# Optimization experiments

Hardware: AMD Instinct MI355X
Metric: run time of the kernel (lower is better)

The kernel has to match this reference:

```python
import jax, jax.numpy as jnp
import numpy as np

N = 20000
E = 320000
NEG_SLOPE = 0.2
BN_EPS = 1e-5


def _segment_softmax(e, dst, n):
    # e: [E, H] attention logits, dst: [E] destination node ids
    m = jax.ops.segment_max(e, dst, num_segments=n)           # [N, H]
    ex = jnp.exp(e - m[dst])                                   # [E, H]
    s = jax.ops.segment_sum(ex, dst, num_segments=n)          # [N, H]
    return ex / s[dst]


def gat_conv(x, src, dst, W, a_src, a_dst, b, heads, out_ch):
    # PyG GATConv (concat=True): h = x @ W reshaped to [N, H, C]
    n = x.shape[0]
    h = (x @ W).reshape(n, heads, out_ch)                      # [N, H, C]
    al_s = jnp.einsum('nhc,hc->nh', h, a_src)                  # [N, H]
    al_d = jnp.einsum('nhc,hc->nh', h, a_dst)
    e = jax.nn.leaky_relu(al_s[src] + al_d[dst], NEG_SLOPE)    # [E, H]
    alpha = _segment_softmax(e, dst, n)                        # [E, H]
    msg = h[src] * alpha[:, :, None]                           # [E, H, C]
    out = jax.ops.segment_sum(msg, dst, num_segments=n)        # [N, H, C]
    return out.reshape(n, heads * out_ch) + b


def batch_norm(x, gamma, beta):
    mu = jnp.mean(x, axis=0)
    var = jnp.mean((x - mu) ** 2, axis=0)  # biased, as torch BN training
    return gamma * (x - mu) * jax.lax.rsqrt(var + BN_EPS) + beta


def setup_inputs() -> dict:
    key = jax.random.key(0)
    ks = jax.random.split(key, 16)
    F_in, H1, C1 = 128, 8, 64
    D = H1 * C1  # 512
    OUT = 2
    def gl(k, shape, fan):
        return jax.random.normal(k, shape, dtype=jnp.float32) / np.sqrt(fan)
    x = jax.random.normal(ks[0], (N, F_in), dtype=jnp.float32)
    edge_index = jax.random.randint(ks[1], (2, E), 0, N, dtype=jnp.int64)
    return {
        'x': x, 'edge_index': edge_index,
        'W1': gl(ks[2], (F_in, H1 * C1), F_in),
        'a1s': gl(ks[3], (H1, C1), C1), 'a1d': gl(ks[4], (H1, C1), C1),
        'b1': jnp.zeros((D,), jnp.float32),
        'W2': gl(ks[5], (D, D), D),
        'a2s': gl(ks[6], (1, D), D), 'a2d': gl(ks[7], (1, D), D),
        'b2': jnp.zeros((D,), jnp.float32),
        'fc1_w': gl(ks[8], (D, D), D), 'fc1_b': jnp.zeros((D,), jnp.float32),
        'g1': jnp.ones((D,), jnp.float32), 'be1': jnp.zeros((D,), jnp.float32),
        'fc2_w': gl(ks[9], (D, D), D), 'fc2_b': jnp.zeros((D,), jnp.float32),
        'g2': jnp.ones((D,), jnp.float32), 'be2': jnp.zeros((D,), jnp.float32),
        'lin_w': gl(ks[10], (D, OUT), D), 'lin_b': jnp.zeros((OUT,), jnp.float32),
    }


def reference(x, edge_index, W1, a1s, a1d, b1, W2, a2s, a2d, b2,
              fc1_w, fc1_b, g1, be1, fc2_w, fc2_b, g2, be2, lin_w, lin_b):
    n = x.shape[0]
    loop = jnp.arange(n, dtype=edge_index.dtype)
    src = jnp.concatenate([edge_index[0], loop])  # add self-loops (PyG default)
    dst = jnp.concatenate([edge_index[1], loop])
    h = gat_conv(x, src, dst, W1, a1s, a1d, b1, heads=8, out_ch=64)
    h = batch_norm(jax.nn.relu(h @ fc1_w + fc1_b), g1, be1)
    h = gat_conv(h, src, dst, W2, a2s, a2d, b2, heads=1, out_ch=512)
    h = batch_norm(jax.nn.relu(h @ fc2_w + fc2_b), g2, be2)
    out = jax.nn.relu(h @ lin_w + lin_b)  # dropout p=0 is identity
    return out
```

## Files before the change

kernel.cpp:

```cpp
#include <hip/hip_runtime.h>
#include <hip/hip_bf16.h>

static constexpr int NN = 20000;
static constexpr int EE = 320000;
static constexpr int ET = EE + NN;
static constexpr int DD = 512;
static constexpr int FIN = 128;

typedef __attribute__((ext_vector_type(8))) short short8;
typedef __attribute__((ext_vector_type(4))) float f32x4;

__device__ __forceinline__ unsigned short f2bf(float f) {
    unsigned u = __float_as_uint(f);
    u += 0x7fffu + ((u >> 16) & 1u);
    return (unsigned short)(u >> 16);
}
__device__ __forceinline__ float bf2f(unsigned short b) {
    return __uint_as_float(((unsigned)b) << 16);
}

__device__ __forceinline__ void async_copy16(short* lds, const unsigned short* g) {
    __builtin_amdgcn_global_load_lds(
        (const __attribute__((address_space(1))) unsigned int*)g,
        (__attribute__((address_space(3))) unsigned int*)lds,
        16, 0, 0);
}

__global__ void init_k(int* __restrict__ deg, int* __restrict__ cursor,
                       const unsigned* __restrict__ ei, int* __restrict__ flag) {
    int i = blockIdx.x * blockDim.x + threadIdx.x;
    if (i < NN) { deg[i] = 1; cursor[i] = 0; }
    if (i == 0) {
        int is64 = 1;
        for (int j = 0; j < 64; ++j)
            if (ei[2 * j + 1] != 0u) { is64 = 0; break; }
        *flag = is64;
    }
}

__global__ void count_deg(const void* __restrict__ ei, const int* __restrict__ flag,
                          int* __restrict__ deg) {
    int i = blockIdx.x * blockDim.x + threadIdx.x;
    if (i >= EE) return;
    int d = (*flag) ? (int)((const long long*)ei)[EE + i] : ((const int*)ei)[EE + i];
    atomicAdd(&deg[d], 1);
}

__global__ void scan_k(const int* __restrict__ deg, int* __restrict__ row_ptr) {
    __shared__ int part[1024];
    int t = threadIdx.x;
    const int CH = (NN + 1023) / 1024;
    int start = t * CH;
    int end = min(start + CH, NN);
    int s = 0;
    for (int i = start; i < end; ++i) s += deg[i];
    part[t] = s;
    __syncthreads();
    for (int off = 1; off < 1024; off <<= 1) {
        int v = 0;
        if (t >= off) v = part[t - off];
        __syncthreads();
        part[t] += v;
        __syncthreads();
    }
    int base = (t == 0) ? 0 : part[t - 1];
    for (int i = start; i < end; ++i) { row_ptr[i] = base; base += deg[i]; }
    if (t == 1023) row_ptr[NN] = part[1023];
}

__global__ void fill_csr(const void* __restrict__ ei, const int* __restrict__ flag,
                         const int* __restrict__ row_ptr, int* __restrict__ cursor,
                         int* __restrict__ csr_src) {
    int e = blockIdx.x * blockDim.x + threadIdx.x;
    if (e >= ET) return;
    int s, d;
    if (e < EE) {
        if (*flag) {
            const long long* p = (const long long*)ei;
            s = (int)p[e]; d = (int)p[EE + e];
        } else {
            const int* p = (const int*)ei;
            s = p[e]; d = p[EE + e];
        }
    } else {
        s = d = e - EE;
    }
    int pos = atomicAdd(&cursor[d], 1);
    csr_src[row_ptr[d] + pos] = s;
}

static constexpr int TBLK = 208;
static constexpr int SZ_X = NN * FIN;
static constexpr int SZ_Z = 2 * 1024 + 2 * NN;
__global__ __launch_bounds__(256) void prep_all_k(
    const float* __restrict__ x, const float* __restrict__ W1,
    const float* __restrict__ fc1, const float* __restrict__ W2,
    const float* __restrict__ fc2,
    unsigned short* __restrict__ xb, unsigned short* __restrict__ W1t,
    unsigned short* __restrict__ fc1t, unsigned short* __restrict__ W2t,
    unsigned short* __restrict__ fc2t,
    float* __restrict__ bnstatA, float* __restrict__ bnstatB,
    float* __restrict__ al_s2, float* __restrict__ al_d2) {
    int b = blockIdx.x;
    if (b < TBLK) {
        __shared__ unsigned short tile[64][65];
        const float* src; unsigned short* dst; int rows, cols;
        if (b < 16)       { src = W1;  dst = W1t;  rows = FIN; cols = DD; }
        else if (b < 80)  { b -= 16;  src = fc1; dst = fc1t; rows = DD; cols = DD; }
        else if (b < 144) { b -= 80;  src = W2;  dst = W2t;  rows = DD; cols = DD; }
        else              { b -= 144; src = fc2; dst = fc2t; rows = DD; cols = DD; }
        int tc = cols / 64;
        int r0 = (b / tc) * 64, c0 = (b % tc) * 64;
        int t = threadIdx.x, lr = t >> 6, lc = t & 63;
#pragma unroll
        for (int p = 0; p < 16; ++p) {
            int r = lr + p * 4;
            tile[r][lc] = f2bf(src[(size_t)(r0 + r) * cols + c0 + lc]);
        }
        __syncthreads();
#pragma unroll
        for (int p = 0; p < 16; ++p) {
            int r = lr + p * 4;
            dst[(size_t)(c0 + r) * rows + r0 + lc] = tile[lc][r];
        }
        return;
    }
    int i = (b - TBLK) * 256 + threadIdx.x;
    if (i < SZ_X) { xb[i] = f2bf(x[i]); return; }
    i -= SZ_X;
    if (i < 1024) { bnstatA[i] = 0.f; return; }
    i -= 1024;
    if (i < 1024) { bnstatB[i] = 0.f; return; }
    i -= 1024;
    if (i < NN) { al_s2[i] = 0.f; return; }
    i -= NN;
    if (i < NN) { al_d2[i] = 0.f; return; }
}

template <int RELU, int HASBIAS, int STATS, int ALS, int H>
__global__ __launch_bounds__(256) void gemm_bf16(const unsigned short* __restrict__ A,
                                                 const unsigned short* __restrict__ Bt,
                                                 const float* __restrict__ bias,
                                                 unsigned short* __restrict__ Cb,
                                                 float* __restrict__ bnstat,
                                                 const float* __restrict__ avs,
                                                 const float* __restrict__ avd,
                                                 float* __restrict__ al_s,
                                                 float* __restrict__ al_d,
                                                 int M, int Nc, int K) {
    int id = blockIdx.x;
    int bm = ((id >> 5) << 3) + (id & 7);
    int bn = (id >> 3) & 3;
    int m0 = bm * 128, n0 = bn * 128;
    if (m0 >= M) return;

    __shared__ short As0[128 * 32], As1[128 * 32];
    __shared__ short Bs0[128 * 32], Bs1[128 * 32];
    int t = threadIdx.x;
    int lane = t & 63, w = t >> 6;
    int wm = w & 1, wn = w >> 1;
    int quad = lane >> 4, mr = lane & 15;
    int lrow = lane >> 2;
    int lcol = (lane & 3) * 8;

    const unsigned short* Ag0 = A + (size_t)(m0 + w * 32 + lrow) * K + lcol;
    const unsigned short* Ag1 = A + (size_t)(m0 + w * 32 + 16 + lrow) * K + lcol;
    const unsigned short* Bg0 = Bt + (size_t)(n0 + w * 32 + lrow) * K + lcol;
    const unsigned short* Bg1 = Bt + (size_t)(n0 + w * 32 + 16 + lrow) * K + lcol;
    short* Al[2][2] = {{&As0[(w * 32) * 32], &As0[(w * 32 + 16) * 32]},
                       {&As1[(w * 32) * 32], &As1[(w * 32 + 16) * 32]}};
    short* Bl[2][2] = {{&Bs0[(w * 32) * 32], &Bs0[(w * 32 + 16) * 32]},
                       {&Bs1[(w * 32) * 32], &Bs1[(w * 32 + 16) * 32]}};

    f32x4 zero = {0.f, 0.f, 0.f, 0.f};
    f32x4 acc[4][4];
#pragma unroll
    for (int i = 0; i < 4; ++i)
#pragma unroll
        for (int j = 0; j < 4; ++j) acc[i][j] = zero;

    for (int k0 = 0; k0 < K; k0 += 64) {
        async_copy16(Al[0][0], Ag0 + k0);
        async_copy16(Al[1][0], Ag0 + k0 + 32);
        async_copy16(Al[0][1], Ag1 + k0);
        async_copy16(Al[1][1], Ag1 + k0 + 32);
        async_copy16(Bl[0][0], Bg0 + k0);
        async_copy16(Bl[1][0], Bg0 + k0 + 32);
        async_copy16(Bl[0][1], Bg1 + k0);
        async_copy16(Bl[1][1], Bg1 + k0 + 32);
        __syncthreads();
#pragma unroll
        for (int kp = 0; kp < 2; ++kp) {
            const short* Sa = kp ? As1 : As0;
            const short* Sb = kp ? Bs1 : Bs0;
            short8 af[4], bfr[4];
#pragma unroll
            for (int i = 0; i < 4; ++i) {
                af[i]  = *(const short8*)(&Sa[(wm * 64 + i * 16 + mr) * 32 + quad * 8]);
                bfr[i] = *(const short8*)(&Sb[(wn * 64 + i * 16 + mr) * 32 + quad * 8]);
            }
#pragma unroll
            for (int i = 0; i < 4; ++i)
#pragma unroll
                for (int j = 0; j < 4; ++j)
                    acc[i][j] = __builtin_amdgcn_mfma_f32_16x16x32_bf16(af[i], bfr[j], acc[i][j], 0, 0, 0);
        }
        __syncthreads();
    }

    float as_j[4], ad_j[4];
    if (ALS) {
#pragma unroll
        for (int j = 0; j < 4; ++j) {
            int n = n0 + wn * 64 + j * 16 + mr;
            as_j[j] = avs[n];
            ad_j[j] = avd[n];
        }
    }
    const int head = (H == 8) ? ((n0 + wn * 64) >> 6) : 0;
    float sj[4] = {0.f, 0.f, 0.f, 0.f}, qj[4] = {0.f, 0.f, 0.f, 0.f};
#pragma unroll
    for (int i = 0; i < 4; ++i) {
        int mb = m0 + wm * 64 + i * 16 + quad * 4;
#pragma unroll
        for (int r = 0; r < 4; ++r) {
            int m = mb + r;
            bool valid = (m < M);
            float ps = 0.f, pd = 0.f;
#pragma unroll
            for (int j = 0; j < 4; ++j) {
                int n = n0 + wn * 64 + j * 16 + mr;
                float v = acc[i][j][r];
                if (HASBIAS) v += bias[n];
                if (RELU) v = fmaxf(v, 0.f);
                unsigned short hb = f2bf(v);
                if (valid) Cb[(size_t)m * Nc + n] = hb;
                if (ALS) {
                    float vv = bf2f(hb);
                    ps += as_j[j] * vv;
                    pd += ad_j[j] * vv;
                }
                if (STATS && valid) { sj[j] += v; qj[j] += v * v; }
            }
            if (ALS) {
                ps += __shfl_xor(ps, 1); pd += __shfl_xor(pd, 1);
                ps += __shfl_xor(ps, 2); pd += __shfl_xor(pd, 2);
                ps += __shfl_xor(ps, 4); pd += __shfl_xor(pd, 4);
                ps += __shfl_xor(ps, 8); pd += __shfl_xor(pd, 8);
                if (mr == 0 && valid) {
                    if (H == 8) { al_s[m * 8 + head] = ps; al_d[m * 8 + head] = pd; }
                    else        { atomicAdd(&al_s[m], ps); atomicAdd(&al_d[m], pd); }
                }
            }
        }
    }
    if (STATS) {
#pragma unroll
        for (int j = 0; j < 4; ++j) {
            float s = sj[j], q = qj[j];
            s += __shfl_xor(s, 16); q += __shfl_xor(q, 16);
            s += __shfl_xor(s, 32); q += __shfl_xor(q, 32);
            if (lane < 16) {
                int n = n0 + wn * 64 + j * 16 + mr;
                atomicAdd(&bnstat[n], s);
                atomicAdd(&bnstat[512 + n], q);
            }
        }
    }
}

template <int H>
__global__ __launch_bounds__(256) void gat_gather_k(const unsigned short* __restrict__ hb,
                                                    const float* __restrict__ al_s,
                                                    const float* __restrict__ al_d,
                                                    const int* __restrict__ row_ptr,
                                                    const int* __restrict__ csr_src,
                                                    const float* __restrict__ bias,
                                                    unsigned short* __restrict__ outb) {
    int t = threadIdx.x;
    int w = t >> 6, lane = t & 63;
    int n = blockIdx.x * 4 + w;
    int beg = row_ptr[n], end = row_ptr[n + 1];
    const int hh = (H == 8) ? (lane >> 3) : 0;
    float ald = al_d[n * H + hh];
    float psum = 0.f;
    float acc[8] = {0.f, 0.f, 0.f, 0.f, 0.f, 0.f, 0.f, 0.f};

    for (int p0 = beg; p0 < end; p0 += 64) {
        int cnt = min(64, end - p0);
        int sv = (p0 + lane < end) ? csr_src[p0 + lane] : 0;
        int p = 0;
        for (; p + 8 <= cnt; p += 8) {
            int sn[8];
#pragma unroll
            for (int u = 0; u < 8; ++u) sn[u] = __shfl(sv, p + u);
            float l[8];
#pragma unroll
            for (int u = 0; u < 8; ++u) l[u] = al_s[sn[u] * H + hh] + ald;
            short8 hv[8];
#pragma unroll
            for (int u = 0; u < 8; ++u)
                hv[u] = *(const short8*)(hb + (size_t)sn[u] * DD + lane * 8);
            float a[8];
#pragma unroll
            for (int u = 0; u < 8; ++u) {
                float x = l[u];
                a[u] = __expf((x > 0.f) ? x : 0.2f * x);
                psum += a[u];
            }
#pragma unroll
            for (int u = 0; u < 8; ++u)
#pragma unroll
                for (int j = 0; j < 8; ++j) acc[j] += a[u] * bf2f((unsigned short)hv[u][j]);
        }
        for (; p < cnt; ++p) {
            int sn0 = __shfl(sv, p);
            float l0 = al_s[sn0 * H + hh] + ald;
            short8 h0 = *(const short8*)(hb + (size_t)sn0 * DD + lane * 8);
            float a0 = __expf((l0 > 0.f) ? l0 : 0.2f * l0);
            psum += a0;
#pragma unroll
            for (int j = 0; j < 8; ++j) acc[j] += a0 * bf2f((unsigned short)h0[j]);
        }
    }
    float inv = 1.0f / psum;
    unsigned short ov[8];
#pragma unroll
    for (int j = 0; j < 8; ++j) ov[j] = f2bf(acc[j] * inv + bias[lane * 8 + j]);
    *(int4*)(outb + (size_t)n * DD + lane * 8) = *(const int4*)ov;
}

__global__ __launch_bounds__(256) void fold1_k(const float* __restrict__ stat,
                                               const float* __restrict__ g,
                                               const float* __restrict__ be,
                                               unsigned short* __restrict__ W2t,
                                               float* __restrict__ bias2) {
    int t = threadIdx.x;
    int n = blockIdx.x * 4 + (t >> 6);
    int lane = t & 63;
    float pb = 0.f;
#pragma unroll
    for (int j = 0; j < 8; ++j) {
        int k = lane * 8 + j;
        float mean = stat[k] * (1.0f / NN);
        float var = stat[512 + k] * (1.0f / NN) - mean * mean;
        float sc = g[k] * rsqrtf(var + 1e-5f);
        float sh = be[k] - mean * sc;
        float wv = bf2f(W2t[n * DD + k]);
        W2t[n * DD + k] = f2bf(sc * wv);
        pb += sh * wv;
    }
    for (int off = 32; off; off >>= 1) pb += __shfl_down(pb, off);
    if (lane == 0) bias2[n] = pb;
}

__global__ void final_linear(const unsigned short* __restrict__ xb,
                             const float* __restrict__ stat, const float* __restrict__ g,
                             const float* __restrict__ be, const float* __restrict__ w,
                             const float* __restrict__ b, float* __restrict__ out) {
    int wave = (blockIdx.x * blockDim.x + threadIdx.x) >> 6;
    int lane = threadIdx.x & 63;
    if (wave >= NN) return;
    short8 hv = *(const short8*)(xb + (size_t)wave * DD + lane * 8);
    float p0 = 0.f, p1 = 0.f;
#pragma unroll
    for (int j = 0; j < 8; ++j) {
        int c = lane * 8 + j;
        float mean = stat[c] * (1.0f / NN);
        float var = stat[512 + c] * (1.0f / NN) - mean * mean;
        float sc = g[c] * rsqrtf(var + 1e-5f);
        float vn = (bf2f((unsigned short)hv[j]) - mean) * sc + be[c];
        p0 += vn * w[2 * c];
        p1 += vn * w[2 * c + 1];
    }
    for (int off = 32; off; off >>= 1) {
        p0 += __shfl_down(p0, off);
        p1 += __shfl_down(p1, off);
    }
    if (lane == 0) {
        out[wave * 2 + 0] = fmaxf(p0 + b[0], 0.f);
        out[wave * 2 + 1] = fmaxf(p1 + b[1], 0.f);
    }
}

extern "C" void kernel_launch(void* const* d_in, const int* in_sizes, int n_in,
                              void* d_out, int out_size, void* d_ws, size_t ws_size,
                              hipStream_t stream) {
    const float* x     = (const float*)d_in[0];
    const void*  ei    = d_in[1];
    const float* W1    = (const float*)d_in[2];
    const float* a1s   = (const float*)d_in[3];
    const float* a1d   = (const float*)d_in[4];
    const float* b1    = (const float*)d_in[5];
    const float* W2    = (const float*)d_in[6];
    const float* a2s   = (const float*)d_in[7];
    const float* a2d   = (const float*)d_in[8];
    const float* b2    = (const float*)d_in[9];
    const float* fc1_w = (const float*)d_in[10];
    const float* fc1_b = (const float*)d_in[11];
    const float* g1    = (const float*)d_in[12];
    const float* be1   = (const float*)d_in[13];
    const float* fc2_w = (const float*)d_in[14];
    const float* fc2_b = (const float*)d_in[15];
    const float* g2    = (const float*)d_in[16];
    const float* be2   = (const float*)d_in[17];
    const float* lin_w = (const float*)d_in[18];
    const float* lin_b = (const float*)d_in[19];
    float* out = (float*)d_out;

    char* ws = (char*)d_ws;
    auto alloc = [&](size_t bytes) {
        void* p = (void*)ws;
        ws += (bytes + 255) & ~size_t(255);
        return p;
    };
    unsigned short* h_bf    = (unsigned short*)alloc((size_t)NN * DD * 2);
    unsigned short* act_bf  = (unsigned short*)alloc((size_t)NN * DD * 2);
    unsigned short* W1t     = (unsigned short*)alloc((size_t)DD * FIN * 2);
    unsigned short* fc1t    = (unsigned short*)alloc((size_t)DD * DD * 2);
    unsigned short* W2t     = (unsigned short*)alloc((size_t)DD * DD * 2);
    unsigned short* fc2t    = (unsigned short*)alloc((size_t)DD * DD * 2);
    float*          al_s    = (float*)alloc((size_t)NN * 8 * 4);
    float*          al_d    = (float*)alloc((size_t)NN * 8 * 4);
    float*          al_s2   = (float*)alloc((size_t)NN * 4);
    float*          al_d2   = (float*)alloc((size_t)NN * 4);
    int*            row_ptr = (int*)alloc((size_t)(NN + 1) * 4);
    int*            deg     = (int*)alloc((size_t)NN * 4);
    int*            cursor  = (int*)alloc((size_t)NN * 4);
    int*            csr_src = (int*)alloc((size_t)ET * 4);
    int*            flag    = (int*)alloc(256);
    float*          bnstatA = (float*)alloc(1024 * 4);
    float*          bnstatB = (float*)alloc(1024 * 4);
    float*          bias2f  = (float*)alloc(512 * 4);

    init_k<<<(NN + 255) / 256, 256, 0, stream>>>(deg, cursor, (const unsigned*)ei, flag);
    count_deg<<<(EE + 255) / 256, 256, 0, stream>>>(ei, flag, deg);
    scan_k<<<1, 1024, 0, stream>>>(deg, row_ptr);
    fill_csr<<<(ET + 255) / 256, 256, 0, stream>>>(ei, flag, row_ptr, cursor, csr_src);

    unsigned short* x_bf = act_bf;
    const int prep_blocks = TBLK + (SZ_X + SZ_Z + 255) / 256;
    prep_all_k<<<prep_blocks, 256, 0, stream>>>(x, W1, fc1_w, W2, fc2_w,
                                                x_bf, W1t, fc1t, W2t, fc2t,
                                                bnstatA, bnstatB, al_s2, al_d2);

    const int GB = 640;

    gemm_bf16<0, 0, 0, 1, 8><<<GB, 256, 0, stream>>>(
        x_bf, W1t, nullptr, h_bf, nullptr, a1s, a1d, al_s, al_d, NN, DD, FIN);
    gat_gather_k<8><<<NN / 4, 256, 0, stream>>>(h_bf, al_s, al_d, row_ptr, csr_src, b1, act_bf);
    gemm_bf16<1, 1, 1, 0, 8><<<GB, 256, 0, stream>>>(
        act_bf, fc1t, fc1_b, h_bf, bnstatA, nullptr, nullptr, nullptr, nullptr, NN, DD, DD);
    fold1_k<<<128, 256, 0, stream>>>(bnstatA, g1, be1, W2t, bias2f);

    gemm_bf16<0, 1, 0, 1, 1><<<GB, 256, 0, stream>>>(
        h_bf, W2t, bias2f, act_bf, nullptr, a2s, a2d, al_s2, al_d2, NN, DD, DD);
    gat_gather_k<1><<<NN / 4, 256, 0, stream>>>(act_bf, al_s2, al_d2, row_ptr, csr_src, b2, h_bf);
    gemm_bf16<1, 1, 1, 0, 8><<<GB, 256, 0, stream>>>(
        h_bf, fc2t, fc2_b, act_bf, bnstatB, nullptr, nullptr, nullptr, nullptr, NN, DD, DD);

    final_linear<<<(NN + 3) / 4, 256, 0, stream>>>(act_bf, bnstatB, g2, be2, lin_w, lin_b, out);
}
```

Before: 367.7 us.

## Bucket CSR neighbors by source-id chunk for gather locality

Builds the CSR so that each destination's neighbor list is partially sorted by source-node chunk (2048-node buckets), using per-(dst,chunk) counts, bases and cursors plus an extra base kernel. The goal is better cache locality in the gather kernels, which read h rows of source nodes. In exchange it adds an extra kernel, more atomics in count_deg, and larger scratch arrays that must be initialized.

```diff
diff --git a/kernel.cpp b/kernel.cpp
--- a/kernel.cpp
+++ b/kernel.cpp
@@ -7,6 +7,9 @@
 static constexpr int DD = 512;
 static constexpr int FIN = 128;
 
+static constexpr int CSH = 11;
+static constexpr int NCH = (NN + (1 << CSH) - 1) >> CSH;
+
 typedef __attribute__((ext_vector_type(8))) short short8;
 typedef __attribute__((ext_vector_type(4))) float f32x4;
 
@@ -26,10 +29,19 @@
         16, 0, 0);
 }
 
-__global__ void init_k(int* __restrict__ deg, int* __restrict__ cursor,
-                       const unsigned* __restrict__ ei, int* __restrict__ flag) {
+__global__ void init_k(int* __restrict__ deg, int* __restrict__ cnt2,
+                       int* __restrict__ cur2, const unsigned* __restrict__ ei,
+                       int* __restrict__ flag) {
     int i = blockIdx.x * blockDim.x + threadIdx.x;
-    if (i < NN) { deg[i] = 1; cursor[i] = 0; }
+    if (i < NN) {
+        deg[i] = 1;
+        int kself = i >> CSH;
+#pragma unroll
+        for (int k = 0; k < NCH; ++k) {
+            cnt2[i * NCH + k] = (k == kself) ? 1 : 0;
+            cur2[i * NCH + k] = 0;
+        }
+    }
     if (i == 0) {
         int is64 = 1;
         for (int j = 0; j < 64; ++j)
@@ -39,11 +51,19 @@
 }
 
 __global__ void count_deg(const void* __restrict__ ei, const int* __restrict__ flag,
-                          int* __restrict__ deg) {
+                          int* __restrict__ deg, int* __restrict__ cnt2) {
     int i = blockIdx.x * blockDim.x + threadIdx.x;
     if (i >= EE) return;
-    int d = (*flag) ? (int)((const long long*)ei)[EE + i] : ((const int*)ei)[EE + i];
+    int s, d;
+    if (*flag) {
+        const long long* p = (const long long*)ei;
+        s = (int)p[i]; d = (int)p[EE + i];
+    } else {
+        const int* p = (const int*)ei;
+        s = p[i]; d = p[EE + i];
+    }
     atomicAdd(&deg[d], 1);
+    atomicAdd(&cnt2[d * NCH + (s >> CSH)], 1);
 }
 
 __global__ void scan_k(const int* __restrict__ deg, int* __restrict__ row_ptr) {
@@ -68,8 +88,20 @@
     if (t == 1023) row_ptr[NN] = part[1023];
 }
 
+__global__ void base_k(const int* __restrict__ row_ptr, const int* __restrict__ cnt2,
+                       int* __restrict__ base2) {
+    int d = blockIdx.x * blockDim.x + threadIdx.x;
+    if (d >= NN) return;
+    int run = row_ptr[d];
+#pragma unroll
+    for (int k = 0; k < NCH; ++k) {
+        base2[d * NCH + k] = run;
+        run += cnt2[d * NCH + k];
+    }
+}
+
 __global__ void fill_csr(const void* __restrict__ ei, const int* __restrict__ flag,
-                         const int* __restrict__ row_ptr, int* __restrict__ cursor,
+                         const int* __restrict__ base2, int* __restrict__ cur2,
                          int* __restrict__ csr_src) {
     int e = blockIdx.x * blockDim.x + threadIdx.x;
     if (e >= ET) return;
@@ -85,8 +117,9 @@
     } else {
         s = d = e - EE;
     }
-    int pos = atomicAdd(&cursor[d], 1);
-    csr_src[row_ptr[d] + pos] = s;
+    int idx2 = d * NCH + (s >> CSH);
+    int pos = atomicAdd(&cur2[idx2], 1);
+    csr_src[base2[idx2] + pos] = s;
 }
 
 static constexpr int TBLK = 208;
@@ -304,8 +337,8 @@
             float a[8];
 #pragma unroll
             for (int u = 0; u < 8; ++u) {
-                float x = l[u];
-                a[u] = __expf((x > 0.f) ? x : 0.2f * x);
+                float xx = l[u];
+                a[u] = __expf((xx > 0.f) ? xx : 0.2f * xx);
                 psum += a[u];
             }
 #pragma unroll
@@ -426,17 +459,20 @@
     float*          al_d2   = (float*)alloc((size_t)NN * 4);
     int*            row_ptr = (int*)alloc((size_t)(NN + 1) * 4);
     int*            deg     = (int*)alloc((size_t)NN * 4);
-    int*            cursor  = (int*)alloc((size_t)NN * 4);
+    int*            cnt2    = (int*)alloc((size_t)NN * NCH * 4);
+    int*            base2   = (int*)alloc((size_t)NN * NCH * 4);
+    int*            cur2    = (int*)alloc((size_t)NN * NCH * 4);
     int*            csr_src = (int*)alloc((size_t)ET * 4);
     int*            flag    = (int*)alloc(256);
     float*          bnstatA = (float*)alloc(1024 * 4);
     float*          bnstatB = (float*)alloc(1024 * 4);
     float*          bias2f  = (float*)alloc(512 * 4);
 
-    init_k<<<(NN + 255) / 256, 256, 0, stream>>>(deg, cursor, (const unsigned*)ei, flag);
-    count_deg<<<(EE + 255) / 256, 256, 0, stream>>>(ei, flag, deg);
+    init_k<<<(NN + 255) / 256, 256, 0, stream>>>(deg, cnt2, cur2, (const unsigned*)ei, flag);
+    count_deg<<<(EE + 255) / 256, 256, 0, stream>>>(ei, flag, deg, cnt2);
     scan_k<<<1, 1024, 0, stream>>>(deg, row_ptr);
-    fill_csr<<<(ET + 255) / 256, 256, 0, stream>>>(ei, flag, row_ptr, cursor, csr_src);
+    base_k<<<(NN + 255) / 256, 256, 0, stream>>>(row_ptr, cnt2, base2);
+    fill_csr<<<(ET + 255) / 256, 256, 0, stream>>>(ei, flag, base2, cur2, csr_src);
 
     unsigned short* x_bf = act_bf;
     const int prep_blocks = TBLK + (SZ_X + SZ_Z + 255) / 256;
```

Measured after the change: 377.1 us. 2.5% more time.
